# Kernel tuning notes

Measured on AMD Instinct MI355X. Metric: run time of the kernel, lower is better.

Reference implementation:

```python
import jax, jax.numpy as jnp
import numpy as np

IN_F = 4096
OUT_F = 4096
RANK = 128  # config.group_size doubles as LoRA rank
B, S = 8, 16


def setup_inputs() -> dict:
    key = jax.random.key(0)
    k_x, k_wq, k_s, k_a, k_b, k_bias = jax.random.split(key, 6)
    x = jax.random.normal(k_x, (B, S, IN_F), dtype=jnp.float32)
    # 4-bit signed quantized weights stored as int8 in torch; int32 here, values in [-8, 7]
    weight_quantized = jax.random.randint(k_wq, (OUT_F, IN_F), -8, 8, dtype=jnp.int32)
    weight_scale = jax.random.uniform(k_s, (OUT_F,), dtype=jnp.float32, minval=0.01, maxval=0.1)
    # kaiming_uniform-ish init for lora_A; lora_B nonzero here so grads flow in tests
    bound = 1.0 / np.sqrt(IN_F)
    lora_A = jax.random.uniform(k_a, (IN_F, RANK), dtype=jnp.float32, minval=-bound, maxval=bound)
    lora_B = jax.random.normal(k_b, (RANK, OUT_F), dtype=jnp.float32) * 0.01
    bias = jax.random.normal(k_bias, (OUT_F,), dtype=jnp.float32) * 0.01
    return {"x": x, "weight_quantized": weight_quantized, "weight_scale": weight_scale,
            "lora_A": lora_A, "lora_B": lora_B, "bias": bias}


def reference(x, weight_quantized, weight_scale, lora_A, lora_B, bias):
    # dequantize: per-output-row scale (out, in)
    weight_dequant = weight_quantized.astype(x.dtype) * weight_scale[:, None]
    # low-rank LoRA update (in, out); square layer so broadcast-add is elementwise
    lora_weight = lora_A @ lora_B
    weight = weight_dequant + lora_weight
    # F.linear: x @ weight.T + bias
    out = jnp.einsum('bsi,oi->bso', x, weight) + bias
    return out
```

## Files before the change

### kernel.cpp

```cpp
#include <hip/hip_runtime.h>
#include <hip/hip_bf16.h>

typedef __attribute__((ext_vector_type(8))) short short8;
typedef __attribute__((ext_vector_type(4))) float f32x4;
using u16 = unsigned short;
using u32 = unsigned int;

#define IN_F 4096
#define OUT_F 4096
#define RANK 128
#define M_TOK 128

typedef const __attribute__((address_space(1))) int* gas_ptr;
typedef __attribute__((address_space(3))) int* las_ptr;

__device__ inline u32 packi(int a, int b) {
    float fa = (float)a, fb = (float)b;
    return (__builtin_bit_cast(u32, fa) >> 16) |
           (__builtin_bit_cast(u32, fb) & 0xFFFF0000u);
}
__device__ inline u32 packf(float a, float b) {
    u32 ua = __builtin_bit_cast(u32, a);
    u32 ub = __builtin_bit_cast(u32, b);
    ua = (ua + 0x7FFFu + ((ua >> 16) & 1u)) >> 16;
    ub = (ub + 0x7FFFu + ((ub >> 16) & 1u));
    return ua | (ub & 0xFFFF0000u);
}
__device__ inline u16 f2bf(float f) {
    u32 u = __builtin_bit_cast(u32, f);
    u = (u + 0x7FFFu + ((u >> 16) & 1u)) >> 16;
    return (u16)u;
}

#define WS_Y 0
#define WS_XB 65536
#define WS_BT (WS_XB + 1048576)
#define WS_AT (WS_BT + 1048576)

__global__ __launch_bounds__(256) void prep0_kernel(
    const float* __restrict__ x, const float* __restrict__ A,
    const float* __restrict__ B, float* __restrict__ outz,
    float* __restrict__ y, u16* __restrict__ xb,
    u16* __restrict__ at, u16* __restrict__ bt) {
    __shared__ float tile[64 * 33];
    int bid = blockIdx.x, tid = threadIdx.x;
    if (bid < 256) {
        const f32x4* xv = (const f32x4*)x;
        int vi = bid * 512 + tid * 2;
        f32x4 a = xv[vi], b = xv[vi + 1];
        union { u32 u[4]; short8 s; } p;
        p.u[0] = packf(a[0], a[1]); p.u[1] = packf(a[2], a[3]);
        p.u[2] = packf(b[0], b[1]); p.u[3] = packf(b[2], b[3]);
        *(short8*)(xb + (size_t)vi * 4) = p.s;
    } else if (bid < 512) {
        int b2 = bid - 256, kt = b2 >> 2, rt = b2 & 3;
        int k0 = kt * 64, r0 = rt * 32;
        for (int u = tid; u < 2048; u += 256) {
            int row = u >> 5, c = u & 31;
            tile[row * 33 + c] = A[(size_t)(k0 + row) * RANK + r0 + c];
        }
        __syncthreads();
        for (int u = tid; u < 2048; u += 256) {
            int rr = u >> 6, k = u & 63;
            at[(size_t)(r0 + rr) * IN_F + k0 + k] = f2bf(tile[k * 33 + rr]);
        }
    } else if (bid < 768) {
        int b2 = bid - 512, rt = b2 >> 7, ot = b2 & 127;
        int r0 = rt * 64, o0 = ot * 32;
        for (int u = tid; u < 2048; u += 256) {
            int row = u >> 5, c = u & 31;
            tile[row * 33 + c] = B[(size_t)(r0 + row) * OUT_F + o0 + c];
        }
        __syncthreads();
        for (int u = tid; u < 2048; u += 256) {
            int oo = u >> 6, k = u & 63;
            bt[(size_t)(o0 + oo) * RANK + r0 + k] = f2bf(tile[k * 33 + oo]);
        }
    } else {
        int idx = (bid - 768) * 256 + tid;
        f32x4 z = {0.f, 0.f, 0.f, 0.f};
        if (idx < 131072) ((f32x4*)outz)[idx] = z;
        else if (idx < 131072 + 4096) ((f32x4*)y)[idx - 131072] = z;
    }
}

__global__ __launch_bounds__(512) void lora_y_kernel(
    const u16* __restrict__ xb, const u16* __restrict__ at,
    float* __restrict__ y) {
    int tid = threadIdx.x, lane = tid & 63, wid = tid >> 6;
    int wm = wid >> 1, wn = wid & 1;
    int col = lane & 15, kg = lane >> 4;
    int rt = blockIdx.x & 3, kq = blockIdx.x >> 2;
    int r = rt * 32 + wn * 16 + col;
    int k0 = kq * 256;
    const u16* xp0 = xb + (size_t)(wm * 32 + col) * IN_F + k0 + kg * 8;
    const u16* xp1 = xp0 + (size_t)16 * IN_F;
    const u16* ap = at + (size_t)r * IN_F + k0 + kg * 8;
    f32x4 acc0 = {0.f, 0.f, 0.f, 0.f}, acc1 = {0.f, 0.f, 0.f, 0.f};
    #pragma unroll
    for (int k = 0; k < 256; k += 32) {
        short8 bf = *(const short8*)(ap + k);
        short8 a0 = *(const short8*)(xp0 + k);
        short8 a1 = *(const short8*)(xp1 + k);
        acc0 = __builtin_amdgcn_mfma_f32_16x16x32_bf16(a0, bf, acc0, 0, 0, 0);
        acc1 = __builtin_amdgcn_mfma_f32_16x16x32_bf16(a1, bf, acc1, 0, 0, 0);
    }
    int rbase = wm * 32 + kg * 4;
    #pragma unroll
    for (int j = 0; j < 4; ++j) {
        atomicAdd(&y[(rbase + j) * RANK + r], acc0[j]);
        atomicAdd(&y[(rbase + j + 16) * RANK + r], acc1[j]);
    }
}

#define KCHUNK 1024
#define KSTEP 64
#define NSTEPS 16

__global__ __launch_bounds__(512) void main_kernel(
    const u16* __restrict__ xb, const int* __restrict__ wq,
    const float* __restrict__ scale, const float* __restrict__ bias,
    const float* __restrict__ y, const u16* __restrict__ bt,
    float* __restrict__ out) {
    __shared__ int lds[2][2048];
    int tid = threadIdx.x, lane = tid & 63, wid = tid >> 6;
    int wm = wid >> 1, wn = wid & 1;
    int col = lane & 15, kg = lane >> 4;
    int nb = blockIdx.x & 127, kq = blockIdx.x >> 7;
    int o0 = nb * 32, k0 = kq * KCHUNK;
    int o = o0 + wn * 16 + col;

    int srow = tid >> 4;
    int skint = 4 * ((tid & 15) ^ (srow & 7));
    const int* sp = wq + (size_t)(o0 + srow) * IN_F + k0 + skint;

    const u16* xp0 = xb + (size_t)(wm * 32 + col) * IN_F + k0 + kg * 8;
    const u16* xp1 = xp0 + (size_t)16 * IN_F;

    int brow = wn * 16 + col;
    int brbyte = brow * 256;
    int bmask = (brow & 7) << 4;

    f32x4 acc0 = {0.f, 0.f, 0.f, 0.f}, acc1 = {0.f, 0.f, 0.f, 0.f};

    auto stage = [&](int buf, int t) {
        __builtin_amdgcn_global_load_lds(
            (gas_ptr)(const void*)(sp + t * KSTEP),
            (las_ptr)(void*)&lds[buf][wid * 256], 16, 0, 0);
    };

    stage(0, 0);
    int cur = 0;
    for (int t = 0; t < NSTEPS; ++t) {
        __syncthreads();
        if (t + 1 < NSTEPS) stage(cur ^ 1, t + 1);
        const char* bb = (const char*)&lds[cur][0] + brbyte;
        int koff = t * KSTEP;
        #pragma unroll
        for (int ks = 0; ks < 2; ++ks) {
            int b0 = ks * 128 + kg * 32;
            int4 wa = *(const int4*)(bb + (b0 ^ bmask));
            int4 wb = *(const int4*)(bb + ((b0 + 16) ^ bmask));
            union { u32 u[4]; short8 s; } bf;
            bf.u[0] = packi(wa.x, wa.y); bf.u[1] = packi(wa.z, wa.w);
            bf.u[2] = packi(wb.x, wb.y); bf.u[3] = packi(wb.z, wb.w);
            short8 a0 = *(const short8*)(xp0 + koff + ks * 32);
            short8 a1 = *(const short8*)(xp1 + koff + ks * 32);
            acc0 = __builtin_amdgcn_mfma_f32_16x16x32_bf16(a0, bf.s, acc0, 0, 0, 0);
            acc1 = __builtin_amdgcn_mfma_f32_16x16x32_bf16(a1, bf.s, acc1, 0, 0, 0);
        }
        __syncthreads();
        cur ^= 1;
    }

    float s = scale[o];
    #pragma unroll
    for (int j = 0; j < 4; ++j) { acc0[j] *= s; acc1[j] *= s; }

    if (kq == 0) {
        const float* yp0 = y + (size_t)(wm * 32 + col) * RANK + kg * 8;
        const float* yp1 = yp0 + 16 * RANK;
        const u16* bp = bt + (size_t)o * RANK + kg * 8;
        #pragma unroll
        for (int ks = 0; ks < RANK; ks += 32) {
            f32x4 ya = *(const f32x4*)(yp0 + ks);
            f32x4 yb = *(const f32x4*)(yp0 + ks + 4);
            f32x4 yc = *(const f32x4*)(yp1 + ks);
            f32x4 yd = *(const f32x4*)(yp1 + ks + 4);
            union { u32 u[4]; short8 s; } af0, af1;
            af0.u[0] = packf(ya[0], ya[1]); af0.u[1] = packf(ya[2], ya[3]);
            af0.u[2] = packf(yb[0], yb[1]); af0.u[3] = packf(yb[2], yb[3]);
            af1.u[0] = packf(yc[0], yc[1]); af1.u[1] = packf(yc[2], yc[3]);
            af1.u[2] = packf(yd[0], yd[1]); af1.u[3] = packf(yd[2], yd[3]);
            short8 bfr = *(const short8*)(bp + ks);
            acc0 = __builtin_amdgcn_mfma_f32_16x16x32_bf16(af0.s, bfr, acc0, 0, 0, 0);
            acc1 = __builtin_amdgcn_mfma_f32_16x16x32_bf16(af1.s, bfr, acc1, 0, 0, 0);
        }
        float bv = bias[o];
        #pragma unroll
        for (int j = 0; j < 4; ++j) { acc0[j] += bv; acc1[j] += bv; }
    }

    int rbase = wm * 32 + kg * 4;
    float* op = out + (size_t)rbase * OUT_F + o;
    #pragma unroll
    for (int j = 0; j < 4; ++j) {
        atomicAdd(op + (size_t)j * OUT_F, acc0[j]);
        atomicAdd(op + (size_t)(j + 16) * OUT_F, acc1[j]);
    }
}

extern "C" void kernel_launch(void* const* d_in, const int* in_sizes, int n_in,
                              void* d_out, int out_size, void* d_ws, size_t ws_size,
                              hipStream_t stream) {
    const float* x = (const float*)d_in[0];
    const int* wq = (const int*)d_in[1];
    const float* scale = (const float*)d_in[2];
    const float* A = (const float*)d_in[3];
    const float* B = (const float*)d_in[4];
    const float* bias = (const float*)d_in[5];
    float* out = (float*)d_out;

    char* ws = (char*)d_ws;
    float* y = (float*)(ws + WS_Y);
    u16* xb = (u16*)(ws + WS_XB);
    u16* bt = (u16*)(ws + WS_BT);
    u16* at = (u16*)(ws + WS_AT);

    prep0_kernel<<<1296, 256, 0, stream>>>(x, A, B, out, y, xb, at, bt);
    lora_y_kernel<<<64, 512, 0, stream>>>(xb, at, y);
    main_kernel<<<512, 512, 0, stream>>>(xb, wq, scale, bias, y, bt, out);
}
```

Baseline: 146.9 us.

## Fuse LoRA-y into prep kernel and stream weights directly from global into registers

The LoRA x@A product now runs inside the prep kernel, reading fp32 x and strided A and converting to bf16 on the fly. This drops the A transpose pass and one kernel launch. Zeroing of y and out moves to hipMemsetAsync calls. The main kernel drops LDS staging of the int32 weights and uses register double-buffered direct global loads with a 64-output by 64-token tile. It adds launch bounds for 4 blocks per CU. Each weight row is now read once per token half, so weight traffic likely doubles, and the strided A reads are uncoalesced.

```diff
diff --git a/kernel.cpp b/kernel.cpp
--- a/kernel.cpp
+++ b/kernel.cpp
@@ -9,10 +9,6 @@
 #define IN_F 4096
 #define OUT_F 4096
 #define RANK 128
-#define M_TOK 128
-
-typedef const __attribute__((address_space(1))) int* gas_ptr;
-typedef __attribute__((address_space(3))) int* las_ptr;
 
 __device__ inline u32 packi(int a, int b) {
     float fa = (float)a, fb = (float)b;
@@ -34,151 +30,136 @@
 
 #define WS_Y 0
 #define WS_XB 65536
-#define WS_BT (WS_XB + 1048576)
-#define WS_AT (WS_BT + 1048576)
-
-__global__ __launch_bounds__(256) void prep0_kernel(
+#define WS_BT (65536 + 1048576)
+
+__global__ __launch_bounds__(512) void prep_kernel(
     const float* __restrict__ x, const float* __restrict__ A,
-    const float* __restrict__ B, float* __restrict__ outz,
-    float* __restrict__ y, u16* __restrict__ xb,
-    u16* __restrict__ at, u16* __restrict__ bt) {
+    const float* __restrict__ B, float* __restrict__ y,
+    u16* __restrict__ xb, u16* __restrict__ bt) {
     __shared__ float tile[64 * 33];
     int bid = blockIdx.x, tid = threadIdx.x;
-    if (bid < 256) {
+    if (bid < 64) {
+        int rt = bid & 3, kq = bid >> 2;
+        int lane = tid & 63, wid = tid >> 6;
+        int wm = wid >> 1, wn = wid & 1;
+        int col = lane & 15, kg = lane >> 4;
+        int r = rt * 32 + wn * 16 + col;
+        int k0 = kq * 256;
+        const float* xq0 = x + (size_t)(wm * 32 + col) * IN_F + k0 + kg * 8;
+        const float* xq1 = xq0 + (size_t)16 * IN_F;
+        const float* ap = A + (size_t)(k0 + kg * 8) * RANK + r;
+        f32x4 acc0 = {0.f, 0.f, 0.f, 0.f}, acc1 = {0.f, 0.f, 0.f, 0.f};
+        #pragma unroll
+        for (int it = 0; it < 8; ++it) {
+            f32x4 xa = *(const f32x4*)(xq0 + it * 32);
+            f32x4 xc = *(const f32x4*)(xq0 + it * 32 + 4);
+            f32x4 xe = *(const f32x4*)(xq1 + it * 32);
+            f32x4 xg = *(const f32x4*)(xq1 + it * 32 + 4);
+            union { u32 u[4]; short8 s; } a0, a1, bf;
+            a0.u[0] = packf(xa[0], xa[1]); a0.u[1] = packf(xa[2], xa[3]);
+            a0.u[2] = packf(xc[0], xc[1]); a0.u[3] = packf(xc[2], xc[3]);
+            a1.u[0] = packf(xe[0], xe[1]); a1.u[1] = packf(xe[2], xe[3]);
+            a1.u[2] = packf(xg[0], xg[1]); a1.u[3] = packf(xg[2], xg[3]);
+            float s0 = ap[(size_t)(it * 32 + 0) * RANK];
+            float s1 = ap[(size_t)(it * 32 + 1) * RANK];
+            float s2 = ap[(size_t)(it * 32 + 2) * RANK];
+            float s3 = ap[(size_t)(it * 32 + 3) * RANK];
+            float s4 = ap[(size_t)(it * 32 + 4) * RANK];
+            float s5 = ap[(size_t)(it * 32 + 5) * RANK];
+            float s6 = ap[(size_t)(it * 32 + 6) * RANK];
+            float s7 = ap[(size_t)(it * 32 + 7) * RANK];
+            bf.u[0] = packf(s0, s1); bf.u[1] = packf(s2, s3);
+            bf.u[2] = packf(s4, s5); bf.u[3] = packf(s6, s7);
+            acc0 = __builtin_amdgcn_mfma_f32_16x16x32_bf16(a0.s, bf.s, acc0, 0, 0, 0);
+            acc1 = __builtin_amdgcn_mfma_f32_16x16x32_bf16(a1.s, bf.s, acc1, 0, 0, 0);
+        }
+        int rbase = wm * 32 + kg * 4;
+        #pragma unroll
+        for (int j = 0; j < 4; ++j) {
+            atomicAdd(&y[(rbase + j) * RANK + r], acc0[j]);
+            atomicAdd(&y[(rbase + j + 16) * RANK + r], acc1[j]);
+        }
+    } else if (bid < 192) {
+        int b2 = bid - 64;
         const f32x4* xv = (const f32x4*)x;
-        int vi = bid * 512 + tid * 2;
+        int vi = b2 * 1024 + tid * 2;
         f32x4 a = xv[vi], b = xv[vi + 1];
         union { u32 u[4]; short8 s; } p;
         p.u[0] = packf(a[0], a[1]); p.u[1] = packf(a[2], a[3]);
         p.u[2] = packf(b[0], b[1]); p.u[3] = packf(b[2], b[3]);
         *(short8*)(xb + (size_t)vi * 4) = p.s;
-    } else if (bid < 512) {
-        int b2 = bid - 256, kt = b2 >> 2, rt = b2 & 3;
-        int k0 = kt * 64, r0 = rt * 32;
-        for (int u = tid; u < 2048; u += 256) {
-            int row = u >> 5, c = u & 31;
-            tile[row * 33 + c] = A[(size_t)(k0 + row) * RANK + r0 + c];
-        }
-        __syncthreads();
-        for (int u = tid; u < 2048; u += 256) {
-            int rr = u >> 6, k = u & 63;
-            at[(size_t)(r0 + rr) * IN_F + k0 + k] = f2bf(tile[k * 33 + rr]);
-        }
-    } else if (bid < 768) {
-        int b2 = bid - 512, rt = b2 >> 7, ot = b2 & 127;
+    } else {
+        int b2 = bid - 192, rt = b2 >> 7, ot = b2 & 127;
         int r0 = rt * 64, o0 = ot * 32;
-        for (int u = tid; u < 2048; u += 256) {
+        for (int u = tid; u < 2048; u += 512) {
             int row = u >> 5, c = u & 31;
             tile[row * 33 + c] = B[(size_t)(r0 + row) * OUT_F + o0 + c];
         }
         __syncthreads();
-        for (int u = tid; u < 2048; u += 256) {
+        for (int u = tid; u < 2048; u += 512) {
             int oo = u >> 6, k = u & 63;
             bt[(size_t)(o0 + oo) * RANK + r0 + k] = f2bf(tile[k * 33 + oo]);
         }
-    } else {
-        int idx = (bid - 768) * 256 + tid;
-        f32x4 z = {0.f, 0.f, 0.f, 0.f};
-        if (idx < 131072) ((f32x4*)outz)[idx] = z;
-        else if (idx < 131072 + 4096) ((f32x4*)y)[idx - 131072] = z;
-    }
-}
-
-__global__ __launch_bounds__(512) void lora_y_kernel(
-    const u16* __restrict__ xb, const u16* __restrict__ at,
-    float* __restrict__ y) {
-    int tid = threadIdx.x, lane = tid & 63, wid = tid >> 6;
-    int wm = wid >> 1, wn = wid & 1;
-    int col = lane & 15, kg = lane >> 4;
-    int rt = blockIdx.x & 3, kq = blockIdx.x >> 2;
-    int r = rt * 32 + wn * 16 + col;
-    int k0 = kq * 256;
-    const u16* xp0 = xb + (size_t)(wm * 32 + col) * IN_F + k0 + kg * 8;
-    const u16* xp1 = xp0 + (size_t)16 * IN_F;
-    const u16* ap = at + (size_t)r * IN_F + k0 + kg * 8;
-    f32x4 acc0 = {0.f, 0.f, 0.f, 0.f}, acc1 = {0.f, 0.f, 0.f, 0.f};
-    #pragma unroll
-    for (int k = 0; k < 256; k += 32) {
-        short8 bf = *(const short8*)(ap + k);
-        short8 a0 = *(const short8*)(xp0 + k);
-        short8 a1 = *(const short8*)(xp1 + k);
-        acc0 = __builtin_amdgcn_mfma_f32_16x16x32_bf16(a0, bf, acc0, 0, 0, 0);
-        acc1 = __builtin_amdgcn_mfma_f32_16x16x32_bf16(a1, bf, acc1, 0, 0, 0);
-    }
-    int rbase = wm * 32 + kg * 4;
-    #pragma unroll
-    for (int j = 0; j < 4; ++j) {
-        atomicAdd(&y[(rbase + j) * RANK + r], acc0[j]);
-        atomicAdd(&y[(rbase + j + 16) * RANK + r], acc1[j]);
     }
 }
 
 #define KCHUNK 1024
-#define KSTEP 64
-#define NSTEPS 16
-
-__global__ __launch_bounds__(512) void main_kernel(
+
+__global__ __launch_bounds__(512, 4) void main_kernel(
     const u16* __restrict__ xb, const int* __restrict__ wq,
     const float* __restrict__ scale, const float* __restrict__ bias,
     const float* __restrict__ y, const u16* __restrict__ bt,
     float* __restrict__ out) {
-    __shared__ int lds[2][2048];
     int tid = threadIdx.x, lane = tid & 63, wid = tid >> 6;
-    int wm = wid >> 1, wn = wid & 1;
+    int wm = wid >> 2, wn = wid & 3;
     int col = lane & 15, kg = lane >> 4;
-    int nb = blockIdx.x & 127, kq = blockIdx.x >> 7;
-    int o0 = nb * 32, k0 = kq * KCHUNK;
-    int o = o0 + wn * 16 + col;
-
-    int srow = tid >> 4;
-    int skint = 4 * ((tid & 15) ^ (srow & 7));
-    const int* sp = wq + (size_t)(o0 + srow) * IN_F + k0 + skint;
-
-    const u16* xp0 = xb + (size_t)(wm * 32 + col) * IN_F + k0 + kg * 8;
+    int bid = blockIdx.x;
+    int ot = bid & 63, mt = (bid >> 6) & 1, kq = bid >> 7;
+    int o = ot * 64 + wn * 16 + col;
+    int m0 = mt * 64 + wm * 32 + col;
+    int k0 = kq * KCHUNK;
+
+    const int* wp = wq + (size_t)o * IN_F + k0 + kg * 8;
+    const u16* xp0 = xb + (size_t)m0 * IN_F + k0 + kg * 8;
     const u16* xp1 = xp0 + (size_t)16 * IN_F;
 
-    int brow = wn * 16 + col;
-    int brbyte = brow * 256;
-    int bmask = (brow & 7) << 4;
-
     f32x4 acc0 = {0.f, 0.f, 0.f, 0.f}, acc1 = {0.f, 0.f, 0.f, 0.f};
 
-    auto stage = [&](int buf, int t) {
-        __builtin_amdgcn_global_load_lds(
-            (gas_ptr)(const void*)(sp + t * KSTEP),
-            (las_ptr)(void*)&lds[buf][wid * 256], 16, 0, 0);
-    };
-
-    stage(0, 0);
-    int cur = 0;
-    for (int t = 0; t < NSTEPS; ++t) {
-        __syncthreads();
-        if (t + 1 < NSTEPS) stage(cur ^ 1, t + 1);
-        const char* bb = (const char*)&lds[cur][0] + brbyte;
-        int koff = t * KSTEP;
-        #pragma unroll
-        for (int ks = 0; ks < 2; ++ks) {
-            int b0 = ks * 128 + kg * 32;
-            int4 wa = *(const int4*)(bb + (b0 ^ bmask));
-            int4 wb = *(const int4*)(bb + ((b0 + 16) ^ bmask));
-            union { u32 u[4]; short8 s; } bf;
-            bf.u[0] = packi(wa.x, wa.y); bf.u[1] = packi(wa.z, wa.w);
-            bf.u[2] = packi(wb.x, wb.y); bf.u[3] = packi(wb.z, wb.w);
-            short8 a0 = *(const short8*)(xp0 + koff + ks * 32);
-            short8 a1 = *(const short8*)(xp1 + koff + ks * 32);
-            acc0 = __builtin_amdgcn_mfma_f32_16x16x32_bf16(a0, bf.s, acc0, 0, 0, 0);
-            acc1 = __builtin_amdgcn_mfma_f32_16x16x32_bf16(a1, bf.s, acc1, 0, 0, 0);
-        }
-        __syncthreads();
-        cur ^= 1;
-    }
+    int4 wva0, wvb0, wva1, wvb1;
+    short8 xv00, xv10, xv01, xv11;
+
+#define LD0(it) { wva0 = *(const int4*)(wp + (it) * 32); \
+                  wvb0 = *(const int4*)(wp + (it) * 32 + 4); \
+                  xv00 = *(const short8*)(xp0 + (it) * 32); \
+                  xv10 = *(const short8*)(xp1 + (it) * 32); }
+#define LD1(it) { wva1 = *(const int4*)(wp + (it) * 32); \
+                  wvb1 = *(const int4*)(wp + (it) * 32 + 4); \
+                  xv01 = *(const short8*)(xp0 + (it) * 32); \
+                  xv11 = *(const short8*)(xp1 + (it) * 32); }
+#define CMP0 { union { u32 u[4]; short8 s; } bf; \
+               bf.u[0] = packi(wva0.x, wva0.y); bf.u[1] = packi(wva0.z, wva0.w); \
+               bf.u[2] = packi(wvb0.x, wvb0.y); bf.u[3] = packi(wvb0.z, wvb0.w); \
+               acc0 = __builtin_amdgcn_mfma_f32_16x16x32_bf16(xv00, bf.s, acc0, 0, 0, 0); \
+               acc1 = __builtin_amdgcn_mfma_f32_16x16x32_bf16(xv10, bf.s, acc1, 0, 0, 0); }
+#define CMP1 { union { u32 u[4]; short8 s; } bf; \
+               bf.u[0] = packi(wva1.x, wva1.y); bf.u[1] = packi(wva1.z, wva1.w); \
+               bf.u[2] = packi(wvb1.x, wvb1.y); bf.u[3] = packi(wvb1.z, wvb1.w); \
+               acc0 = __builtin_amdgcn_mfma_f32_16x16x32_bf16(xv01, bf.s, acc0, 0, 0, 0); \
+               acc1 = __builtin_amdgcn_mfma_f32_16x16x32_bf16(xv11, bf.s, acc1, 0, 0, 0); }
+
+    LD0(0); LD1(1);
+    for (int it2 = 0; it2 < 15; ++it2) {
+        CMP0; LD0(2 * it2 + 2);
+        CMP1; LD1(2 * it2 + 3);
+    }
+    CMP0; CMP1;
 
     float s = scale[o];
     #pragma unroll
     for (int j = 0; j < 4; ++j) { acc0[j] *= s; acc1[j] *= s; }
 
     if (kq == 0) {
-        const float* yp0 = y + (size_t)(wm * 32 + col) * RANK + kg * 8;
+        const float* yp0 = y + (size_t)m0 * RANK + kg * 8;
         const float* yp1 = yp0 + 16 * RANK;
         const u16* bp = bt + (size_t)o * RANK + kg * 8;
         #pragma unroll
@@ -201,7 +182,7 @@
         for (int j = 0; j < 4; ++j) { acc0[j] += bv; acc1[j] += bv; }
     }
 
-    int rbase = wm * 32 + kg * 4;
+    int rbase = mt * 64 + wm * 32 + kg * 4;
     float* op = out + (size_t)rbase * OUT_F + o;
     #pragma unroll
     for (int j = 0; j < 4; ++j) {
@@ -225,9 +206,9 @@
     float* y = (float*)(ws + WS_Y);
     u16* xb = (u16*)(ws + WS_XB);
     u16* bt = (u16*)(ws + WS_BT);
-    u16* at = (u16*)(ws + WS_AT);
-
-    prep0_kernel<<<1296, 256, 0, stream>>>(x, A, B, out, y, xb, at, bt);
-    lora_y_kernel<<<64, 512, 0, stream>>>(xb, at, y);
+
+    hipMemsetAsync(y, 0, 65536, stream);
+    hipMemsetAsync(out, 0, (size_t)out_size * sizeof(float), stream);
+    prep_kernel<<<448, 512, 0, stream>>>(x, A, B, y, xb, bt);
     main_kernel<<<512, 512, 0, stream>>>(xb, wq, scale, bias, y, bt, out);
 }
```

Result: slower. 169.0 us (+15.0%).

## Pre-convert quantized weights to bf16 MFMA-fragment layout and simplify main GEMM

Applied to the files above, without the earlier changes.

Adds a pass inside the second prep kernel that converts the int32 quantized weights into bf16 stored in the exact per-lane MFMA fragment order. When the workspace is large enough, the main GEMM then streams fragments with one contiguous load per step, with no LDS staging, no barriers and no in-loop int-to-bf16 conversion. Otherwise a fallback kernel reads int32 weights directly from global memory. Both paths use a new 64x64 block tiling, and the LoRA-y computation is folded into the same launch as the weight conversion. In exchange, the conversion pass adds an extra 32 MB write and read of the bf16 weights on every call, and its benefit depends on a workspace-size check.

```diff
diff --git a/kernel.cpp b/kernel.cpp
--- a/kernel.cpp
+++ b/kernel.cpp
@@ -9,10 +9,6 @@
 #define IN_F 4096
 #define OUT_F 4096
 #define RANK 128
-#define M_TOK 128
-
-typedef const __attribute__((address_space(1))) int* gas_ptr;
-typedef __attribute__((address_space(3))) int* las_ptr;
 
 __device__ inline u32 packi(int a, int b) {
     float fa = (float)a, fb = (float)b;
@@ -36,149 +32,117 @@
 #define WS_XB 65536
 #define WS_BT (WS_XB + 1048576)
 #define WS_AT (WS_BT + 1048576)
-
-__global__ __launch_bounds__(256) void prep0_kernel(
+#define WS_WQB (WS_AT + 1048576)
+#define WS_NEED (WS_WQB + (size_t)33554432)
+
+__global__ __launch_bounds__(512) void prep1_kernel(
     const float* __restrict__ x, const float* __restrict__ A,
     const float* __restrict__ B, float* __restrict__ outz,
     float* __restrict__ y, u16* __restrict__ xb,
     u16* __restrict__ at, u16* __restrict__ bt) {
     __shared__ float tile[64 * 33];
     int bid = blockIdx.x, tid = threadIdx.x;
-    if (bid < 256) {
+    if (bid < 128) {
         const f32x4* xv = (const f32x4*)x;
-        int vi = bid * 512 + tid * 2;
+        int vi = bid * 1024 + tid * 2;
         f32x4 a = xv[vi], b = xv[vi + 1];
         union { u32 u[4]; short8 s; } p;
         p.u[0] = packf(a[0], a[1]); p.u[1] = packf(a[2], a[3]);
         p.u[2] = packf(b[0], b[1]); p.u[3] = packf(b[2], b[3]);
         *(short8*)(xb + (size_t)vi * 4) = p.s;
-    } else if (bid < 512) {
-        int b2 = bid - 256, kt = b2 >> 2, rt = b2 & 3;
+    } else if (bid < 384) {
+        int b2 = bid - 128, kt = b2 >> 2, rt = b2 & 3;
         int k0 = kt * 64, r0 = rt * 32;
-        for (int u = tid; u < 2048; u += 256) {
+        for (int u = tid; u < 2048; u += 512) {
             int row = u >> 5, c = u & 31;
             tile[row * 33 + c] = A[(size_t)(k0 + row) * RANK + r0 + c];
         }
         __syncthreads();
-        for (int u = tid; u < 2048; u += 256) {
+        for (int u = tid; u < 2048; u += 512) {
             int rr = u >> 6, k = u & 63;
             at[(size_t)(r0 + rr) * IN_F + k0 + k] = f2bf(tile[k * 33 + rr]);
         }
-    } else if (bid < 768) {
-        int b2 = bid - 512, rt = b2 >> 7, ot = b2 & 127;
+    } else if (bid < 640) {
+        int b2 = bid - 384, rt = b2 >> 7, ot = b2 & 127;
         int r0 = rt * 64, o0 = ot * 32;
-        for (int u = tid; u < 2048; u += 256) {
+        for (int u = tid; u < 2048; u += 512) {
             int row = u >> 5, c = u & 31;
             tile[row * 33 + c] = B[(size_t)(r0 + row) * OUT_F + o0 + c];
         }
         __syncthreads();
-        for (int u = tid; u < 2048; u += 256) {
+        for (int u = tid; u < 2048; u += 512) {
             int oo = u >> 6, k = u & 63;
             bt[(size_t)(o0 + oo) * RANK + r0 + k] = f2bf(tile[k * 33 + oo]);
         }
+    } else if (bid < 896) {
+        int idx = (bid - 640) * 512 + tid;
+        f32x4 z = {0.f, 0.f, 0.f, 0.f};
+        ((f32x4*)outz)[idx] = z;
     } else {
-        int idx = (bid - 768) * 256 + tid;
+        int idx = (bid - 896) * 512 + tid;
         f32x4 z = {0.f, 0.f, 0.f, 0.f};
-        if (idx < 131072) ((f32x4*)outz)[idx] = z;
-        else if (idx < 131072 + 4096) ((f32x4*)y)[idx - 131072] = z;
-    }
-}
-
-__global__ __launch_bounds__(512) void lora_y_kernel(
+        ((f32x4*)y)[idx] = z;
+    }
+}
+
+__global__ __launch_bounds__(512) void prep2_kernel(
     const u16* __restrict__ xb, const u16* __restrict__ at,
-    float* __restrict__ y) {
-    int tid = threadIdx.x, lane = tid & 63, wid = tid >> 6;
-    int wm = wid >> 1, wn = wid & 1;
-    int col = lane & 15, kg = lane >> 4;
-    int rt = blockIdx.x & 3, kq = blockIdx.x >> 2;
-    int r = rt * 32 + wn * 16 + col;
-    int k0 = kq * 256;
-    const u16* xp0 = xb + (size_t)(wm * 32 + col) * IN_F + k0 + kg * 8;
-    const u16* xp1 = xp0 + (size_t)16 * IN_F;
-    const u16* ap = at + (size_t)r * IN_F + k0 + kg * 8;
-    f32x4 acc0 = {0.f, 0.f, 0.f, 0.f}, acc1 = {0.f, 0.f, 0.f, 0.f};
-    #pragma unroll
-    for (int k = 0; k < 256; k += 32) {
-        short8 bf = *(const short8*)(ap + k);
-        short8 a0 = *(const short8*)(xp0 + k);
-        short8 a1 = *(const short8*)(xp1 + k);
-        acc0 = __builtin_amdgcn_mfma_f32_16x16x32_bf16(a0, bf, acc0, 0, 0, 0);
-        acc1 = __builtin_amdgcn_mfma_f32_16x16x32_bf16(a1, bf, acc1, 0, 0, 0);
-    }
-    int rbase = wm * 32 + kg * 4;
-    #pragma unroll
-    for (int j = 0; j < 4; ++j) {
-        atomicAdd(&y[(rbase + j) * RANK + r], acc0[j]);
-        atomicAdd(&y[(rbase + j + 16) * RANK + r], acc1[j]);
-    }
-}
-
-#define KCHUNK 1024
-#define KSTEP 64
-#define NSTEPS 16
-
-__global__ __launch_bounds__(512) void main_kernel(
-    const u16* __restrict__ xb, const int* __restrict__ wq,
+    float* __restrict__ y, const int* __restrict__ wq,
+    u16* __restrict__ wqb) {
+    int bid = blockIdx.x, tid = threadIdx.x;
+    int lane = tid & 63, wid = tid >> 6;
+    if (bid < 64) {
+        int wm = wid >> 1, wn = wid & 1;
+        int col = lane & 15, kg = lane >> 4;
+        int rt = bid & 3, kq = bid >> 2;
+        int r = rt * 32 + wn * 16 + col;
+        int k0 = kq * 256;
+        const u16* xp0 = xb + (size_t)(wm * 32 + col) * IN_F + k0 + kg * 8;
+        const u16* xp1 = xp0 + (size_t)16 * IN_F;
+        const u16* ap = at + (size_t)r * IN_F + k0 + kg * 8;
+        f32x4 acc0 = {0.f, 0.f, 0.f, 0.f}, acc1 = {0.f, 0.f, 0.f, 0.f};
+        #pragma unroll
+        for (int k = 0; k < 256; k += 32) {
+            short8 bf = *(const short8*)(ap + k);
+            short8 a0 = *(const short8*)(xp0 + k);
+            short8 a1 = *(const short8*)(xp1 + k);
+            acc0 = __builtin_amdgcn_mfma_f32_16x16x32_bf16(a0, bf, acc0, 0, 0, 0);
+            acc1 = __builtin_amdgcn_mfma_f32_16x16x32_bf16(a1, bf, acc1, 0, 0, 0);
+        }
+        int rbase = wm * 32 + kg * 4;
+        #pragma unroll
+        for (int j = 0; j < 4; ++j) {
+            atomicAdd(&y[(rbase + j) * RANK + r], acc0[j]);
+            atomicAdd(&y[(rbase + j + 16) * RANK + r], acc1[j]);
+        }
+    } else {
+        int r = (bid - 64) * 8 + wid;
+        int ntile = r >> 4, col = r & 15;
+        const int* rp = wq + (size_t)r * IN_F + lane * 8;
+        u16* dp = wqb + (size_t)ntile * 65536 + (size_t)(lane >> 2) * 512 +
+                  (size_t)((lane & 3) * 16 + col) * 8;
+        #pragma unroll
+        for (int i = 0; i < 8; ++i) {
+            int4 wa = *(const int4*)(rp + i * 512);
+            int4 wb = *(const int4*)(rp + i * 512 + 4);
+            union { u32 u[4]; short8 s; } p;
+            p.u[0] = packi(wa.x, wa.y); p.u[1] = packi(wa.z, wa.w);
+            p.u[2] = packi(wb.x, wb.y); p.u[3] = packi(wb.z, wb.w);
+            *(short8*)(dp + (size_t)i * 16 * 512) = p.s;
+        }
+    }
+}
+
+__device__ inline void epilogue(
+    f32x4& acc0, f32x4& acc1, int o, int m0, int kq, int rbase,
     const float* __restrict__ scale, const float* __restrict__ bias,
     const float* __restrict__ y, const u16* __restrict__ bt,
-    float* __restrict__ out) {
-    __shared__ int lds[2][2048];
-    int tid = threadIdx.x, lane = tid & 63, wid = tid >> 6;
-    int wm = wid >> 1, wn = wid & 1;
-    int col = lane & 15, kg = lane >> 4;
-    int nb = blockIdx.x & 127, kq = blockIdx.x >> 7;
-    int o0 = nb * 32, k0 = kq * KCHUNK;
-    int o = o0 + wn * 16 + col;
-
-    int srow = tid >> 4;
-    int skint = 4 * ((tid & 15) ^ (srow & 7));
-    const int* sp = wq + (size_t)(o0 + srow) * IN_F + k0 + skint;
-
-    const u16* xp0 = xb + (size_t)(wm * 32 + col) * IN_F + k0 + kg * 8;
-    const u16* xp1 = xp0 + (size_t)16 * IN_F;
-
-    int brow = wn * 16 + col;
-    int brbyte = brow * 256;
-    int bmask = (brow & 7) << 4;
-
-    f32x4 acc0 = {0.f, 0.f, 0.f, 0.f}, acc1 = {0.f, 0.f, 0.f, 0.f};
-
-    auto stage = [&](int buf, int t) {
-        __builtin_amdgcn_global_load_lds(
-            (gas_ptr)(const void*)(sp + t * KSTEP),
-            (las_ptr)(void*)&lds[buf][wid * 256], 16, 0, 0);
-    };
-
-    stage(0, 0);
-    int cur = 0;
-    for (int t = 0; t < NSTEPS; ++t) {
-        __syncthreads();
-        if (t + 1 < NSTEPS) stage(cur ^ 1, t + 1);
-        const char* bb = (const char*)&lds[cur][0] + brbyte;
-        int koff = t * KSTEP;
-        #pragma unroll
-        for (int ks = 0; ks < 2; ++ks) {
-            int b0 = ks * 128 + kg * 32;
-            int4 wa = *(const int4*)(bb + (b0 ^ bmask));
-            int4 wb = *(const int4*)(bb + ((b0 + 16) ^ bmask));
-            union { u32 u[4]; short8 s; } bf;
-            bf.u[0] = packi(wa.x, wa.y); bf.u[1] = packi(wa.z, wa.w);
-            bf.u[2] = packi(wb.x, wb.y); bf.u[3] = packi(wb.z, wb.w);
-            short8 a0 = *(const short8*)(xp0 + koff + ks * 32);
-            short8 a1 = *(const short8*)(xp1 + koff + ks * 32);
-            acc0 = __builtin_amdgcn_mfma_f32_16x16x32_bf16(a0, bf.s, acc0, 0, 0, 0);
-            acc1 = __builtin_amdgcn_mfma_f32_16x16x32_bf16(a1, bf.s, acc1, 0, 0, 0);
-        }
-        __syncthreads();
-        cur ^= 1;
-    }
-
+    float* __restrict__ out, int kg) {
     float s = scale[o];
     #pragma unroll
     for (int j = 0; j < 4; ++j) { acc0[j] *= s; acc1[j] *= s; }
-
     if (kq == 0) {
-        const float* yp0 = y + (size_t)(wm * 32 + col) * RANK + kg * 8;
+        const float* yp0 = y + (size_t)m0 * RANK + kg * 8;
         const float* yp1 = yp0 + 16 * RANK;
         const u16* bp = bt + (size_t)o * RANK + kg * 8;
         #pragma unroll
@@ -200,14 +164,78 @@
         #pragma unroll
         for (int j = 0; j < 4; ++j) { acc0[j] += bv; acc1[j] += bv; }
     }
-
-    int rbase = wm * 32 + kg * 4;
     float* op = out + (size_t)rbase * OUT_F + o;
     #pragma unroll
     for (int j = 0; j < 4; ++j) {
         atomicAdd(op + (size_t)j * OUT_F, acc0[j]);
         atomicAdd(op + (size_t)(j + 16) * OUT_F, acc1[j]);
     }
+}
+
+__global__ __launch_bounds__(512) void main_wqb_kernel(
+    const u16* __restrict__ xb, const u16* __restrict__ wqb,
+    const float* __restrict__ scale, const float* __restrict__ bias,
+    const float* __restrict__ y, const u16* __restrict__ bt,
+    float* __restrict__ out) {
+    int tid = threadIdx.x, lane = tid & 63, wid = tid >> 6;
+    int wm = wid >> 2, wn = wid & 3;
+    int col = lane & 15, kg = lane >> 4;
+    int bid = blockIdx.x;
+    int ot = bid & 63, mt = (bid >> 6) & 1, kq = bid >> 7;
+    int nt = ot * 4 + wn;
+    int o = nt * 16 + col;
+    int m0 = mt * 64 + wm * 32 + col;
+
+    const u16* fp = wqb + (size_t)nt * 65536 + (size_t)kq * 32 * 512 + lane * 8;
+    const u16* xp0 = xb + (size_t)m0 * IN_F + kq * 1024 + kg * 8;
+    const u16* xp1 = xp0 + (size_t)16 * IN_F;
+
+    f32x4 acc0 = {0.f, 0.f, 0.f, 0.f}, acc1 = {0.f, 0.f, 0.f, 0.f};
+    #pragma unroll 8
+    for (int kc = 0; kc < 32; ++kc) {
+        short8 bf = *(const short8*)(fp + kc * 512);
+        short8 a0 = *(const short8*)(xp0 + kc * 32);
+        short8 a1 = *(const short8*)(xp1 + kc * 32);
+        acc0 = __builtin_amdgcn_mfma_f32_16x16x32_bf16(a0, bf, acc0, 0, 0, 0);
+        acc1 = __builtin_amdgcn_mfma_f32_16x16x32_bf16(a1, bf, acc1, 0, 0, 0);
+    }
+    int rbase = mt * 64 + wm * 32 + kg * 4;
+    epilogue(acc0, acc1, o, m0, kq, rbase, scale, bias, y, bt, out, kg);
+}
+
+#define KCHUNK 1024
+__global__ __launch_bounds__(512, 4) void main_direct_kernel(
+    const u16* __restrict__ xb, const int* __restrict__ wq,
+    const float* __restrict__ scale, const float* __restrict__ bias,
+    const float* __restrict__ y, const u16* __restrict__ bt,
+    float* __restrict__ out) {
+    int tid = threadIdx.x, lane = tid & 63, wid = tid >> 6;
+    int wm = wid >> 2, wn = wid & 3;
+    int col = lane & 15, kg = lane >> 4;
+    int bid = blockIdx.x;
+    int ot = bid & 63, mt = (bid >> 6) & 1, kq = bid >> 7;
+    int o = ot * 64 + wn * 16 + col;
+    int m0 = mt * 64 + wm * 32 + col;
+    int k0 = kq * KCHUNK;
+
+    const int* wp = wq + (size_t)o * IN_F + k0 + kg * 8;
+    const u16* xp0 = xb + (size_t)m0 * IN_F + k0 + kg * 8;
+    const u16* xp1 = xp0 + (size_t)16 * IN_F;
+
+    f32x4 acc0 = {0.f, 0.f, 0.f, 0.f}, acc1 = {0.f, 0.f, 0.f, 0.f};
+    for (int it = 0; it < 32; ++it) {
+        int4 wa = *(const int4*)(wp + it * 32);
+        int4 wb = *(const int4*)(wp + it * 32 + 4);
+        union { u32 u[4]; short8 s; } bf;
+        bf.u[0] = packi(wa.x, wa.y); bf.u[1] = packi(wa.z, wa.w);
+        bf.u[2] = packi(wb.x, wb.y); bf.u[3] = packi(wb.z, wb.w);
+        short8 a0 = *(const short8*)(xp0 + it * 32);
+        short8 a1 = *(const short8*)(xp1 + it * 32);
+        acc0 = __builtin_amdgcn_mfma_f32_16x16x32_bf16(a0, bf.s, acc0, 0, 0, 0);
+        acc1 = __builtin_amdgcn_mfma_f32_16x16x32_bf16(a1, bf.s, acc1, 0, 0, 0);
+    }
+    int rbase = mt * 64 + wm * 32 + kg * 4;
+    epilogue(acc0, acc1, o, m0, kq, rbase, scale, bias, y, bt, out, kg);
 }
 
 extern "C" void kernel_launch(void* const* d_in, const int* in_sizes, int n_in,
@@ -226,8 +254,15 @@
     u16* xb = (u16*)(ws + WS_XB);
     u16* bt = (u16*)(ws + WS_BT);
     u16* at = (u16*)(ws + WS_AT);
-
-    prep0_kernel<<<1296, 256, 0, stream>>>(x, A, B, out, y, xb, at, bt);
-    lora_y_kernel<<<64, 512, 0, stream>>>(xb, at, y);
-    main_kernel<<<512, 512, 0, stream>>>(xb, wq, scale, bias, y, bt, out);
-}
+    u16* wqb = (u16*)(ws + WS_WQB);
+
+    bool big = ws_size >= WS_NEED;
+
+    prep1_kernel<<<904, 512, 0, stream>>>(x, A, B, out, y, xb, at, bt);
+    prep2_kernel<<<big ? 576 : 64, 512, 0, stream>>>(xb, at, y, wq, wqb);
+    if (big) {
+        main_wqb_kernel<<<512, 512, 0, stream>>>(xb, wqb, scale, bias, y, bt, out);
+    } else {
+        main_direct_kernel<<<512, 512, 0, stream>>>(xb, wq, scale, bias, y, bt, out);
+    }
+}
```

After: 169.7 us. 15.5% more time.
